# Kernel optimization log

Measured on AMD Instinct MI355X. Metric: run time of the kernel, lower is better.

## Reference

```python
import jax, jax.numpy as jnp
import numpy as np

T, B, D, H = 4096, 4, 1024, 8
EPS = 1e-5


def _ln(z, g, b):
    m = jnp.mean(z, axis=-1, keepdims=True)
    v = jnp.mean((z - m) ** 2, axis=-1, keepdims=True)
    return (z - m) * jax.lax.rsqrt(v + EPS) * g + b


def setup_inputs() -> dict:
    key = jax.random.key(0)
    ks = jax.random.split(key, 8)
    s = 0.02
    return {
        "x": jax.random.normal(ks[0], (T, B, D), dtype=jnp.float32),
        "norm_w": jnp.ones((D,), jnp.float32),
        "norm_b": jnp.zeros((D,), jnp.float32),
        "tnorm_w": jnp.ones((D,), jnp.float32),
        "tnorm_b": jnp.zeros((D,), jnp.float32),
        "Wq": jax.random.normal(ks[1], (D, D), jnp.float32) * s,
        "bq": jnp.zeros((D,), jnp.float32),
        "Wk": jax.random.normal(ks[2], (D, D), jnp.float32) * s,
        "bk": jnp.zeros((D,), jnp.float32),
        "Wv": jax.random.normal(ks[3], (D, D), jnp.float32) * s,
        "bv": jnp.zeros((D,), jnp.float32),
    }


def reference(x, norm_w, norm_b, tnorm_w, tnorm_b, Wq, bq, Wk, bk, Wv, bv):
    # x: (T, B, D) -> (B, T, D), matching torch x.permute(1, 0, 2)
    xb = jnp.transpose(x, (1, 0, 2))
    b, t, d = xb.shape
    hd = d // H
    xn = _ln(xb, norm_w, norm_b)          # query branch norm
    xtn = _ln(xb, tnorm_w, tnorm_b)       # key/value branch norm (text_norm applied to x)
    q = (xn @ Wq.T + bq).reshape(b, t, H, hd)
    k = (xtn @ Wk.T + bk).reshape(b, t, H, hd)
    v = (xtn @ Wv.T + bv).reshape(b, t, H, hd)
    q = jax.nn.softmax(q, axis=-1)        # softmax over head-dim
    k = jax.nn.softmax(k, axis=1)         # softmax over time
    # kv state: (B, H, hd, hd)
    att = jnp.einsum('bthd,bthl->bhdl', k, v)
    y = jnp.einsum('bthd,bhdl->bthl', q, att).reshape(b, t, d)
    return y  # original forward returns y directly (proj_out/dropout unused)
```

## Files before the change

kernel.cpp:

```cpp
#include <hip/hip_runtime.h>
#include <cstdint>

#define T_LEN 4096
#define BATCH 4
#define DIM   1024
#define NH    8
#define HDIM  128
#define ROWS  16384

typedef __bf16 bf16x8 __attribute__((ext_vector_type(8)));
typedef float  f32x4  __attribute__((ext_vector_type(4)));

__device__ __forceinline__ unsigned short f2bf(float f) {
  union { float f; unsigned u; } a; a.f = f;
  unsigned u = a.u;
  u += 0x7fff + ((u >> 16) & 1);
  return (unsigned short)(u >> 16);
}
__device__ __forceinline__ float bf2f(unsigned short h) {
  union { unsigned u; float f; } a; a.u = ((unsigned)h) << 16;
  return a.f;
}

__device__ __forceinline__ void gld_lds16(const unsigned short* g, unsigned short* l) {
  __builtin_amdgcn_global_load_lds(
      (const __attribute__((address_space(1))) unsigned int*)g,
      (__attribute__((address_space(3))) unsigned int*)l, 16, 0, 0);
}

__global__ __launch_bounds__(256) void lnw_kernel(
    const float* __restrict__ x, const float* __restrict__ nw, const float* __restrict__ nb,
    const float* __restrict__ tw, const float* __restrict__ tb,
    unsigned short* __restrict__ xn, unsigned short* __restrict__ xtn,
    const float* __restrict__ Wq, const float* __restrict__ Wk, const float* __restrict__ Wv,
    unsigned short* __restrict__ wbf) {
  int tid = threadIdx.x;
  if (blockIdx.x >= ROWS) {
    int i4 = (blockIdx.x - ROWS) * 256 + tid;
    int w = i4 >> 18;
    const float* src = (w == 0) ? Wq : (w == 1 ? Wk : Wv);
    float4 v = ((const float4*)src)[i4 & 262143];
    union { unsigned short u[4]; uint2 d; } o;
    o.u[0] = f2bf(v.x); o.u[1] = f2bf(v.y); o.u[2] = f2bf(v.z); o.u[3] = f2bf(v.w);
    ((uint2*)wbf)[i4] = o.d;
    return;
  }
  int row = blockIdx.x;
  int t = row >> 2, b = row & 3;
  const float4 v = ((const float4*)(x + (size_t)row * DIM))[tid];
  float s  = v.x + v.y + v.z + v.w;
  float s2 = v.x*v.x + v.y*v.y + v.z*v.z + v.w*v.w;
#pragma unroll
  for (int o = 32; o; o >>= 1) { s += __shfl_xor(s, o); s2 += __shfl_xor(s2, o); }
  __shared__ float red[8];
  int wv = tid >> 6;
  if ((tid & 63) == 0) { red[wv] = s; red[4 + wv] = s2; }
  __syncthreads();
  s  = red[0] + red[1] + red[2] + red[3];
  s2 = red[4] + red[5] + red[6] + red[7];
  float mean = s * (1.0f / DIM);
  float var  = s2 * (1.0f / DIM) - mean * mean;
  float rstd = rsqrtf(var + 1e-5f);
  size_t orow = ((size_t)b * T_LEN + t) * DIM;
  int c0 = tid * 4;
  float xv[4] = {v.x, v.y, v.z, v.w};
  union { unsigned short u[4]; uint2 d; } o1, o2;
#pragma unroll
  for (int j = 0; j < 4; ++j) {
    int c = c0 + j;
    float xh = (xv[j] - mean) * rstd;
    o1.u[j] = f2bf(xh * nw[c] + nb[c]);
    o2.u[j] = f2bf(xh * tw[c] + tb[c]);
  }
  *(uint2*)(xn  + orow + c0) = o1.d;
  *(uint2*)(xtn + orow + c0) = o2.d;
}

__global__ __launch_bounds__(512, 4) void qkv_gemm(
    const unsigned short* __restrict__ xn, const unsigned short* __restrict__ xtn,
    const unsigned short* __restrict__ wbf,
    const float* __restrict__ bq, const float* __restrict__ bk, const float* __restrict__ bv,
    unsigned short* __restrict__ qo, unsigned short* __restrict__ ko, unsigned short* __restrict__ vo,
    float* __restrict__ Zk) {
  int z = blockIdx.z;
  const unsigned short* A = (z == 0) ? xn : xtn;
  const unsigned short* W = wbf + (size_t)z * DIM * DIM;
  const float* bias = (z == 0) ? bq : (z == 1 ? bk : bv);
  unsigned short* outp = (z == 0) ? qo : (z == 1 ? ko : vo);

  int m0 = blockIdx.x * 256;
  int n0 = blockIdx.y * 128;

  __shared__ __align__(16) unsigned short lds[24576];

  int tid = threadIdx.x;
  int wave = tid >> 6, lane = tid & 63;
  int wr = wave >> 1, wc = wave & 1;
  int wm = wr * 64, wn = wc * 64;
  int l16 = lane & 15, kq = lane >> 4;
  int rs = (kq ^ ((l16 >> 1) & 3)) * 8;

  int arow = tid >> 2;
  int achk = (tid & 3) ^ ((tid >> 3) & 3);
  const unsigned short* Ag = A + (size_t)(m0 + arow) * DIM + achk * 8;
  const unsigned short* Wg = W + (size_t)(n0 + arow) * DIM + achk * 8;

  f32x4 acc[4][4] = {};

  auto stage = [&](int tt, int sb) {
    int kt = tt * 32;
    gld_lds16(Ag + kt,                     lds + sb + wave * 512);
    gld_lds16(Ag + (size_t)128 * DIM + kt, lds + sb + 4096 + wave * 512);
    gld_lds16(Wg + kt,                     lds + sb + 8192 + wave * 512);
  };

  stage(0, 0);
  stage(1, 12288);

  for (int t = 0; t < 32; ++t) {
    int sb = (t & 1) ? 12288 : 0;
    const unsigned short* As = lds + sb;
    const unsigned short* Bs = lds + sb + 8192;

    if (t < 31) asm volatile("s_waitcnt vmcnt(3)" ::: "memory");
    else        asm volatile("s_waitcnt vmcnt(0)" ::: "memory");
    __builtin_amdgcn_sched_barrier(0);
    __builtin_amdgcn_s_barrier();
    __builtin_amdgcn_sched_barrier(0);

    bf16x8 fa[4], fb[4];
#pragma unroll
    for (int i = 0; i < 4; ++i) {
      fa[i] = *(const bf16x8*)(As + (wm + i * 16 + l16) * 32 + rs);
      fb[i] = *(const bf16x8*)(Bs + (wn + i * 16 + l16) * 32 + rs);
    }
#pragma unroll
    for (int i = 0; i < 4; ++i)
#pragma unroll
      for (int j = 0; j < 4; ++j)
        acc[i][j] = __builtin_amdgcn_mfma_f32_16x16x32_bf16(fa[i], fb[j], acc[i][j], 0, 0, 0);

    __builtin_amdgcn_sched_barrier(0);
    __builtin_amdgcn_s_barrier();
    __builtin_amdgcn_sched_barrier(0);
    if (t < 30) stage(t + 2, sb);
    __builtin_amdgcn_sched_barrier(0);
  }

#pragma unroll
  for (int j = 0; j < 4; ++j) {
    float bc = bias[n0 + wn + j * 16 + l16];
#pragma unroll
    for (int i = 0; i < 4; ++i)
#pragma unroll
      for (int r = 0; r < 4; ++r) acc[i][j][r] += bc;
  }

  if (z == 0) {
    float* redm = (float*)lds;
    float* reds = redm + 512;
#pragma unroll
    for (int i = 0; i < 4; ++i) {
#pragma unroll
      for (int r = 0; r < 4; ++r) {
        float pm = acc[i][0][r];
#pragma unroll
        for (int j = 1; j < 4; ++j) pm = fmaxf(pm, acc[i][j][r]);
        pm = fmaxf(pm, __shfl_xor(pm, 1));
        pm = fmaxf(pm, __shfl_xor(pm, 2));
        pm = fmaxf(pm, __shfl_xor(pm, 4));
        pm = fmaxf(pm, __shfl_xor(pm, 8));
        float ps = 0.0f;
#pragma unroll
        for (int j = 0; j < 4; ++j) ps += __expf(acc[i][j][r] - pm);
        ps += __shfl_xor(ps, 1);
        ps += __shfl_xor(ps, 2);
        ps += __shfl_xor(ps, 4);
        ps += __shfl_xor(ps, 8);
        if (l16 == 0) {
          int row = wm + i * 16 + kq * 4 + r;
          redm[row * 2 + wc] = pm;
          reds[row * 2 + wc] = ps;
        }
      }
    }
    __syncthreads();
#pragma unroll
    for (int i = 0; i < 4; ++i) {
#pragma unroll
      for (int r = 0; r < 4; ++r) {
        int row = wm + i * 16 + kq * 4 + r;
        float ma = redm[row * 2], mb = redm[row * 2 + 1];
        float sa = reds[row * 2], sb2 = reds[row * 2 + 1];
        float M = fmaxf(ma, mb);
        float inv = 1.0f / (sa * __expf(ma - M) + sb2 * __expf(mb - M));
        size_t gr = (size_t)(m0 + row) * DIM;
#pragma unroll
        for (int j = 0; j < 4; ++j) {
          int col = n0 + wn + j * 16 + l16;
          outp[gr + col] = f2bf(__expf(acc[i][j][r] - M) * inv);
        }
      }
    }
  } else {
    int b = m0 >> 12;
    int tb = m0 & 4095;
    unsigned short* obase = outp + (size_t)b * DIM * T_LEN + tb;
    bool doExp = (z == 1);
    float zs[4] = {0.0f, 0.0f, 0.0f, 0.0f};
#pragma unroll
    for (int j = 0; j < 4; ++j) {
      int col = n0 + wn + j * 16 + l16;
      unsigned short* cp = obase + (size_t)col * T_LEN;
#pragma unroll
      for (int i = 0; i < 4; ++i) {
        int t0 = wm + i * 16 + kq * 4;
        union { unsigned short u[4]; uint2 d; } o;
#pragma unroll
        for (int r = 0; r < 4; ++r) {
          float val = acc[i][j][r];
          if (doExp) { val = __expf(val); zs[j] += val; }
          o.u[r] = f2bf(val);
        }
        *(uint2*)(cp + t0) = o.d;
      }
    }
    if (doExp) {
#pragma unroll
      for (int j = 0; j < 4; ++j) {
        zs[j] += __shfl_xor(zs[j], 16);
        zs[j] += __shfl_xor(zs[j], 32);
        if (kq == 0) {
          int col = n0 + wn + j * 16 + l16;
          atomicAdd(Zk + b * DIM + col, zs[j]);
        }
      }
    }
  }
}

__global__ __launch_bounds__(256) void att_gemm(
    const unsigned short* __restrict__ vT, const unsigned short* __restrict__ ksmT,
    float* __restrict__ slabs) {
  int kc = blockIdx.x;
  int bh = blockIdx.y;
  const unsigned short* Arow = vT   + (size_t)bh * HDIM * T_LEN;
  const unsigned short* Brow = ksmT + (size_t)bh * HDIM * T_LEN;
  __shared__ __align__(16) unsigned short As[128 * 64];
  __shared__ __align__(16) unsigned short Bs[128 * 64];
  int tid = threadIdx.x;
  int wave = tid >> 6, lane = tid & 63;
  int wm = (wave >> 1) * 64, wn = (wave & 1) * 64;
  int l16 = lane & 15, kq = lane >> 4;
  int swz = l16 & 7;
  int srow = tid >> 3;
  int skk = (((tid & 7) ^ ((tid >> 3) & 7)) * 8);
  const unsigned short* Ag = Arow + (size_t)srow * T_LEN + skk;
  const unsigned short* Bg = Brow + (size_t)srow * T_LEN + skk;
  unsigned short* Al = As + wave * 512;
  unsigned short* Bl = Bs + wave * 512;
  f32x4 acc[4][4] = {};
  int kbeg = kc * 256;
  for (int kt = kbeg; kt < kbeg + 256; kt += 64) {
#pragma unroll
    for (int p = 0; p < 4; ++p) {
      gld_lds16(Ag + (size_t)(p * 32) * T_LEN + kt, Al + p * 2048);
      gld_lds16(Bg + (size_t)(p * 32) * T_LEN + kt, Bl + p * 2048);
    }
    __syncthreads();
#pragma unroll
    for (int ks4 = 0; ks4 < 2; ++ks4) {
      int coff = (((kq + ks4 * 4) ^ swz) * 8);
      bf16x8 fa[4], fb[4];
#pragma unroll
      for (int i = 0; i < 4; ++i) {
        fa[i] = *(const bf16x8*)(As + (wm + i * 16 + l16) * 64 + coff);
        fb[i] = *(const bf16x8*)(Bs + (wn + i * 16 + l16) * 64 + coff);
      }
#pragma unroll
      for (int i = 0; i < 4; ++i)
#pragma unroll
        for (int j = 0; j < 4; ++j)
          acc[i][j] = __builtin_amdgcn_mfma_f32_16x16x32_bf16(fa[i], fb[j], acc[i][j], 0, 0, 0);
    }
    __syncthreads();
  }
  float* op = slabs + ((size_t)kc * 32 + bh) * 16384;
#pragma unroll
  for (int j = 0; j < 4; ++j) {
    int col = wn + j * 16 + l16;
#pragma unroll
    for (int i = 0; i < 4; ++i) {
      int rb = wm + i * 16 + kq * 4;
#pragma unroll
      for (int r = 0; r < 4; ++r)
        op[(size_t)(rb + r) * 128 + col] = acc[i][j][r];
    }
  }
}

__global__ __launch_bounds__(256) void attcvt(
    const float* __restrict__ slabs, const float* __restrict__ Zk,
    unsigned short* __restrict__ attbf) {
  int idx = blockIdx.x * 256 + threadIdx.x;
  int bh = idx >> 14;
  int b = bh >> 3, h = bh & 7;
  int d = idx & 127;
  float s = 0.0f;
#pragma unroll
  for (int kc = 0; kc < 16; ++kc) s += slabs[(size_t)kc * 524288 + idx];
  float zv = Zk[b * DIM + h * HDIM + d];
  attbf[idx] = f2bf(s / zv);
}

__global__ __launch_bounds__(256) void y_gemm(
    const unsigned short* __restrict__ qsm, const unsigned short* __restrict__ attbf,
    float* __restrict__ out) {
  int h = blockIdx.y;
  int m0t = blockIdx.x * 128;
  int b = m0t >> 12;
  int bh = b * 8 + h;
  const unsigned short* Brow = attbf + (size_t)bh * 16384;
  __shared__ __align__(16) unsigned short As[128 * 64];
  __shared__ __align__(16) unsigned short Bs[128 * 64];
  int tid = threadIdx.x;
  int wave = tid >> 6, lane = tid & 63;
  int wm = (wave >> 1) * 64, wn = (wave & 1) * 64;
  int l16 = lane & 15, kq = lane >> 4;
  int swz = l16 & 7;
  int srow = tid >> 3;
  int skk = (((tid & 7) ^ ((tid >> 3) & 7)) * 8);
  const unsigned short* Ag = qsm + (size_t)(m0t + srow) * DIM + h * HDIM + skk;
  const unsigned short* Bg = Brow + (size_t)srow * HDIM + skk;
  unsigned short* Al = As + wave * 512;
  unsigned short* Bl = Bs + wave * 512;
  f32x4 acc[4][4] = {};
  for (int kt = 0; kt < HDIM; kt += 64) {
#pragma unroll
    for (int p = 0; p < 4; ++p) {
      gld_lds16(Ag + (size_t)(p * 32) * DIM + kt, Al + p * 2048);
      gld_lds16(Bg + (size_t)(p * 32) * HDIM + kt, Bl + p * 2048);
    }
    __syncthreads();
#pragma unroll
    for (int ks4 = 0; ks4 < 2; ++ks4) {
      int coff = (((kq + ks4 * 4) ^ swz) * 8);
      bf16x8 fa[4], fb[4];
#pragma unroll
      for (int i = 0; i < 4; ++i) {
        fa[i] = *(const bf16x8*)(As + (wm + i * 16 + l16) * 64 + coff);
        fb[i] = *(const bf16x8*)(Bs + (wn + i * 16 + l16) * 64 + coff);
      }
#pragma unroll
      for (int i = 0; i < 4; ++i)
#pragma unroll
        for (int j = 0; j < 4; ++j)
          acc[i][j] = __builtin_amdgcn_mfma_f32_16x16x32_bf16(fa[i], fb[j], acc[i][j], 0, 0, 0);
    }
    __syncthreads();
  }
#pragma unroll
  for (int j = 0; j < 4; ++j) {
    int col = wn + j * 16 + l16;
#pragma unroll
    for (int i = 0; i < 4; ++i) {
      int rb = wm + i * 16 + kq * 4;
#pragma unroll
      for (int r = 0; r < 4; ++r)
        out[(size_t)(m0t + rb + r) * DIM + h * HDIM + col] = acc[i][j][r];
    }
  }
}

extern "C" void kernel_launch(void* const* d_in, const int* in_sizes, int n_in,
                              void* d_out, int out_size, void* d_ws, size_t ws_size,
                              hipStream_t stream) {
  const float* x  = (const float*)d_in[0];
  const float* nw = (const float*)d_in[1];
  const float* nb = (const float*)d_in[2];
  const float* tw = (const float*)d_in[3];
  const float* tb = (const float*)d_in[4];
  const float* Wq = (const float*)d_in[5];
  const float* bq = (const float*)d_in[6];
  const float* Wk = (const float*)d_in[7];
  const float* bk = (const float*)d_in[8];
  const float* Wv = (const float*)d_in[9];
  const float* bv = (const float*)d_in[10];
  float* out = (float*)d_out;

  char* ws = (char*)d_ws;
  unsigned short* xn   = (unsigned short*)(ws);
  unsigned short* xtn  = (unsigned short*)(ws + 33554432);
  unsigned short* q    = (unsigned short*)(ws + 67108864);
  unsigned short* ksmT = (unsigned short*)(ws + 100663296);
  unsigned short* vT   = (unsigned short*)(ws + 134217728);
  unsigned short* wbf  = (unsigned short*)(ws + 167772160);
  unsigned short* attbf= (unsigned short*)(ws + 176160768);
  float* Zk            = (float*)(ws + 177209344);
  float* slabs         = (float*)(ws);

  (void)hipMemsetAsync(Zk, 0, BATCH * DIM * 4, stream);
  lnw_kernel<<<ROWS + 3072, 256, 0, stream>>>(x, nw, nb, tw, tb, xn, xtn, Wq, Wk, Wv, wbf);
  qkv_gemm<<<dim3(64, 8, 3), 512, 0, stream>>>(xn, xtn, wbf, bq, bk, bv, q, ksmT, vT, Zk);
  att_gemm<<<dim3(16, 32), 256, 0, stream>>>(vT, ksmT, slabs);
  attcvt<<<2048, 256, 0, stream>>>(slabs, Zk, attbf);
  y_gemm<<<dim3(128, 8), 256, 0, stream>>>(q, attbf, out);
}
```

Measured before the change: 317.3 us.

## Fuse Q projection and softmax into the y GEMM, drop q round-trip

```diff
diff --git a/kernel.cpp b/kernel.cpp
--- a/kernel.cpp
+++ b/kernel.cpp
@@ -76,17 +76,15 @@
   *(uint2*)(xtn + orow + c0) = o2.d;
 }
 
-__global__ __launch_bounds__(512, 4) void qkv_gemm(
-    const unsigned short* __restrict__ xn, const unsigned short* __restrict__ xtn,
-    const unsigned short* __restrict__ wbf,
-    const float* __restrict__ bq, const float* __restrict__ bk, const float* __restrict__ bv,
-    unsigned short* __restrict__ qo, unsigned short* __restrict__ ko, unsigned short* __restrict__ vo,
+__global__ __launch_bounds__(512, 4) void kv_gemm(
+    const unsigned short* __restrict__ xtn, const unsigned short* __restrict__ wbf,
+    const float* __restrict__ bk, const float* __restrict__ bv,
+    unsigned short* __restrict__ ko, unsigned short* __restrict__ vo,
     float* __restrict__ Zk) {
-  int z = blockIdx.z;
-  const unsigned short* A = (z == 0) ? xn : xtn;
-  const unsigned short* W = wbf + (size_t)z * DIM * DIM;
-  const float* bias = (z == 0) ? bq : (z == 1 ? bk : bv);
-  unsigned short* outp = (z == 0) ? qo : (z == 1 ? ko : vo);
+  int zz = blockIdx.z + 1;
+  const unsigned short* W = wbf + (size_t)zz * DIM * DIM;
+  const float* bias = (zz == 1) ? bk : bv;
+  unsigned short* outp = (zz == 1) ? ko : vo;
 
   int m0 = blockIdx.x * 256;
   int n0 = blockIdx.y * 128;
@@ -102,7 +100,7 @@
 
   int arow = tid >> 2;
   int achk = (tid & 3) ^ ((tid >> 3) & 3);
-  const unsigned short* Ag = A + (size_t)(m0 + arow) * DIM + achk * 8;
+  const unsigned short* Ag = xtn + (size_t)(m0 + arow) * DIM + achk * 8;
   const unsigned short* Wg = W + (size_t)(n0 + arow) * DIM + achk * 8;
 
   f32x4 acc[4][4] = {};
@@ -156,84 +154,36 @@
       for (int r = 0; r < 4; ++r) acc[i][j][r] += bc;
   }
 
-  if (z == 0) {
-    float* redm = (float*)lds;
-    float* reds = redm + 512;
-#pragma unroll
-    for (int i = 0; i < 4; ++i) {
+  int b = m0 >> 12;
+  int tb = m0 & 4095;
+  unsigned short* obase = outp + (size_t)b * DIM * T_LEN + tb;
+  bool doExp = (zz == 1);
+  float zs[4] = {0.0f, 0.0f, 0.0f, 0.0f};
+#pragma unroll
+  for (int j = 0; j < 4; ++j) {
+    int col = n0 + wn + j * 16 + l16;
+    unsigned short* cp = obase + (size_t)col * T_LEN;
+#pragma unroll
+    for (int i = 0; i < 4; ++i) {
+      int t0 = wm + i * 16 + kq * 4;
+      union { unsigned short u[4]; uint2 d; } o;
 #pragma unroll
       for (int r = 0; r < 4; ++r) {
-        float pm = acc[i][0][r];
-#pragma unroll
-        for (int j = 1; j < 4; ++j) pm = fmaxf(pm, acc[i][j][r]);
-        pm = fmaxf(pm, __shfl_xor(pm, 1));
-        pm = fmaxf(pm, __shfl_xor(pm, 2));
-        pm = fmaxf(pm, __shfl_xor(pm, 4));
-        pm = fmaxf(pm, __shfl_xor(pm, 8));
-        float ps = 0.0f;
-#pragma unroll
-        for (int j = 0; j < 4; ++j) ps += __expf(acc[i][j][r] - pm);
-        ps += __shfl_xor(ps, 1);
-        ps += __shfl_xor(ps, 2);
-        ps += __shfl_xor(ps, 4);
-        ps += __shfl_xor(ps, 8);
-        if (l16 == 0) {
-          int row = wm + i * 16 + kq * 4 + r;
-          redm[row * 2 + wc] = pm;
-          reds[row * 2 + wc] = ps;
-        }
-      }
-    }
-    __syncthreads();
-#pragma unroll
-    for (int i = 0; i < 4; ++i) {
-#pragma unroll
-      for (int r = 0; r < 4; ++r) {
-        int row = wm + i * 16 + kq * 4 + r;
-        float ma = redm[row * 2], mb = redm[row * 2 + 1];
-        float sa = reds[row * 2], sb2 = reds[row * 2 + 1];
-        float M = fmaxf(ma, mb);
-        float inv = 1.0f / (sa * __expf(ma - M) + sb2 * __expf(mb - M));
-        size_t gr = (size_t)(m0 + row) * DIM;
-#pragma unroll
-        for (int j = 0; j < 4; ++j) {
-          int col = n0 + wn + j * 16 + l16;
-          outp[gr + col] = f2bf(__expf(acc[i][j][r] - M) * inv);
-        }
-      }
-    }
-  } else {
-    int b = m0 >> 12;
-    int tb = m0 & 4095;
-    unsigned short* obase = outp + (size_t)b * DIM * T_LEN + tb;
-    bool doExp = (z == 1);
-    float zs[4] = {0.0f, 0.0f, 0.0f, 0.0f};
+        float val = acc[i][j][r];
+        if (doExp) { val = __expf(val); zs[j] += val; }
+        o.u[r] = f2bf(val);
+      }
+      *(uint2*)(cp + t0) = o.d;
+    }
+  }
+  if (doExp) {
 #pragma unroll
     for (int j = 0; j < 4; ++j) {
-      int col = n0 + wn + j * 16 + l16;
-      unsigned short* cp = obase + (size_t)col * T_LEN;
-#pragma unroll
-      for (int i = 0; i < 4; ++i) {
-        int t0 = wm + i * 16 + kq * 4;
-        union { unsigned short u[4]; uint2 d; } o;
-#pragma unroll
-        for (int r = 0; r < 4; ++r) {
-          float val = acc[i][j][r];
-          if (doExp) { val = __expf(val); zs[j] += val; }
-          o.u[r] = f2bf(val);
-        }
-        *(uint2*)(cp + t0) = o.d;
-      }
-    }
-    if (doExp) {
-#pragma unroll
-      for (int j = 0; j < 4; ++j) {
-        zs[j] += __shfl_xor(zs[j], 16);
-        zs[j] += __shfl_xor(zs[j], 32);
-        if (kq == 0) {
-          int col = n0 + wn + j * 16 + l16;
-          atomicAdd(Zk + b * DIM + col, zs[j]);
-        }
+      zs[j] += __shfl_xor(zs[j], 16);
+      zs[j] += __shfl_xor(zs[j], 32);
+      if (kq == 0) {
+        int col = n0 + wn + j * 16 + l16;
+        atomicAdd(Zk + b * DIM + col, zs[j]);
       }
     }
   }
@@ -260,8 +210,8 @@
   unsigned short* Al = As + wave * 512;
   unsigned short* Bl = Bs + wave * 512;
   f32x4 acc[4][4] = {};
-  int kbeg = kc * 256;
-  for (int kt = kbeg; kt < kbeg + 256; kt += 64) {
+  int kbeg = kc * 512;
+  for (int kt = kbeg; kt < kbeg + 512; kt += 64) {
 #pragma unroll
     for (int p = 0; p < 4; ++p) {
       gld_lds16(Ag + (size_t)(p * 32) * T_LEN + kt, Al + p * 2048);
@@ -308,66 +258,184 @@
   int d = idx & 127;
   float s = 0.0f;
 #pragma unroll
-  for (int kc = 0; kc < 16; ++kc) s += slabs[(size_t)kc * 524288 + idx];
+  for (int kc = 0; kc < 8; ++kc) s += slabs[(size_t)kc * 524288 + idx];
   float zv = Zk[b * DIM + h * HDIM + d];
   attbf[idx] = f2bf(s / zv);
 }
 
-__global__ __launch_bounds__(256) void y_gemm(
-    const unsigned short* __restrict__ qsm, const unsigned short* __restrict__ attbf,
+__global__ __launch_bounds__(512) void qy_gemm(
+    const unsigned short* __restrict__ xn, const unsigned short* __restrict__ wbf,
+    const float* __restrict__ bq, const unsigned short* __restrict__ attbf,
     float* __restrict__ out) {
-  int h = blockIdx.y;
-  int m0t = blockIdx.x * 128;
-  int b = m0t >> 12;
+  int m0 = blockIdx.x * 256;
+  int h  = blockIdx.y;
+  int n0 = h * HDIM;
+  int b  = m0 >> 12;
   int bh = b * 8 + h;
-  const unsigned short* Brow = attbf + (size_t)bh * 16384;
-  __shared__ __align__(16) unsigned short As[128 * 64];
-  __shared__ __align__(16) unsigned short Bs[128 * 64];
+
+  __shared__ __align__(16) unsigned short lds[24576];
+
   int tid = threadIdx.x;
   int wave = tid >> 6, lane = tid & 63;
-  int wm = (wave >> 1) * 64, wn = (wave & 1) * 64;
+  int wr = wave >> 1, wc = wave & 1;
+  int wm = wr * 64, wn = wc * 64;
   int l16 = lane & 15, kq = lane >> 4;
-  int swz = l16 & 7;
-  int srow = tid >> 3;
-  int skk = (((tid & 7) ^ ((tid >> 3) & 7)) * 8);
-  const unsigned short* Ag = qsm + (size_t)(m0t + srow) * DIM + h * HDIM + skk;
-  const unsigned short* Bg = Brow + (size_t)srow * HDIM + skk;
-  unsigned short* Al = As + wave * 512;
-  unsigned short* Bl = Bs + wave * 512;
+  int rs = (kq ^ ((l16 >> 1) & 3)) * 8;
+
+  int arow = tid >> 2;
+  int achk = (tid & 3) ^ ((tid >> 3) & 3);
+  const unsigned short* Ag = xn + (size_t)(m0 + arow) * DIM + achk * 8;
+  const unsigned short* Wg = wbf + (size_t)(n0 + arow) * DIM + achk * 8;
+
   f32x4 acc[4][4] = {};
-  for (int kt = 0; kt < HDIM; kt += 64) {
-#pragma unroll
-    for (int p = 0; p < 4; ++p) {
-      gld_lds16(Ag + (size_t)(p * 32) * DIM + kt, Al + p * 2048);
-      gld_lds16(Bg + (size_t)(p * 32) * HDIM + kt, Bl + p * 2048);
+
+  auto stage = [&](int tt, int sb) {
+    int kt = tt * 32;
+    gld_lds16(Ag + kt,                     lds + sb + wave * 512);
+    gld_lds16(Ag + (size_t)128 * DIM + kt, lds + sb + 4096 + wave * 512);
+    gld_lds16(Wg + kt,                     lds + sb + 8192 + wave * 512);
+  };
+
+  stage(0, 0);
+  stage(1, 12288);
+
+  for (int t = 0; t < 32; ++t) {
+    int sb = (t & 1) ? 12288 : 0;
+    const unsigned short* As = lds + sb;
+    const unsigned short* Bs = lds + sb + 8192;
+
+    if (t < 31) asm volatile("s_waitcnt vmcnt(3)" ::: "memory");
+    else        asm volatile("s_waitcnt vmcnt(0)" ::: "memory");
+    __builtin_amdgcn_sched_barrier(0);
+    __builtin_amdgcn_s_barrier();
+    __builtin_amdgcn_sched_barrier(0);
+
+    bf16x8 fa[4], fb[4];
+#pragma unroll
+    for (int i = 0; i < 4; ++i) {
+      fa[i] = *(const bf16x8*)(As + (wm + i * 16 + l16) * 32 + rs);
+      fb[i] = *(const bf16x8*)(Bs + (wn + i * 16 + l16) * 32 + rs);
+    }
+#pragma unroll
+    for (int i = 0; i < 4; ++i)
+#pragma unroll
+      for (int j = 0; j < 4; ++j)
+        acc[i][j] = __builtin_amdgcn_mfma_f32_16x16x32_bf16(fa[i], fb[j], acc[i][j], 0, 0, 0);
+
+    __builtin_amdgcn_sched_barrier(0);
+    __builtin_amdgcn_s_barrier();
+    __builtin_amdgcn_sched_barrier(0);
+    if (t < 30) stage(t + 2, sb);
+    __builtin_amdgcn_sched_barrier(0);
+  }
+
+#pragma unroll
+  for (int j = 0; j < 4; ++j) {
+    float bc = bq[n0 + wn + j * 16 + l16];
+#pragma unroll
+    for (int i = 0; i < 4; ++i)
+#pragma unroll
+      for (int r = 0; r < 4; ++r) acc[i][j][r] += bc;
+  }
+
+  int wmy = (wave >> 2) * 64, wny = (wave & 3) * 32;
+  bf16x8 fby[2][4];
+#pragma unroll
+  for (int jy = 0; jy < 2; ++jy)
+#pragma unroll
+    for (int ks = 0; ks < 4; ++ks) {
+      int ncol = wny + jy * 16 + l16;
+      fby[jy][ks] = *(const bf16x8*)(attbf + (size_t)bh * 16384 + ncol * 128 + ks * 32 + kq * 8);
+    }
+
+  {
+    float* redm = (float*)lds;
+    float* reds = redm + 512;
+#pragma unroll
+    for (int i = 0; i < 4; ++i) {
+#pragma unroll
+      for (int r = 0; r < 4; ++r) {
+        float pm = acc[i][0][r];
+#pragma unroll
+        for (int j = 1; j < 4; ++j) pm = fmaxf(pm, acc[i][j][r]);
+        pm = fmaxf(pm, __shfl_xor(pm, 1));
+        pm = fmaxf(pm, __shfl_xor(pm, 2));
+        pm = fmaxf(pm, __shfl_xor(pm, 4));
+        pm = fmaxf(pm, __shfl_xor(pm, 8));
+        float ps = 0.0f;
+#pragma unroll
+        for (int j = 0; j < 4; ++j) ps += __expf(acc[i][j][r] - pm);
+        ps += __shfl_xor(ps, 1);
+        ps += __shfl_xor(ps, 2);
+        ps += __shfl_xor(ps, 4);
+        ps += __shfl_xor(ps, 8);
+        if (l16 == 0) {
+          int row = wm + i * 16 + kq * 4 + r;
+          redm[row * 2 + wc] = pm;
+          reds[row * 2 + wc] = ps;
+        }
+      }
     }
     __syncthreads();
 #pragma unroll
-    for (int ks4 = 0; ks4 < 2; ++ks4) {
-      int coff = (((kq + ks4 * 4) ^ swz) * 8);
-      bf16x8 fa[4], fb[4];
-#pragma unroll
-      for (int i = 0; i < 4; ++i) {
-        fa[i] = *(const bf16x8*)(As + (wm + i * 16 + l16) * 64 + coff);
-        fb[i] = *(const bf16x8*)(Bs + (wn + i * 16 + l16) * 64 + coff);
-      }
+    for (int i = 0; i < 4; ++i) {
+#pragma unroll
+      for (int r = 0; r < 4; ++r) {
+        int row = wm + i * 16 + kq * 4 + r;
+        float ma = redm[row * 2], mb = redm[row * 2 + 1];
+        float sa = reds[row * 2], sb2 = reds[row * 2 + 1];
+        float M = fmaxf(ma, mb);
+        float inv = 1.0f / (sa * __expf(ma - M) + sb2 * __expf(mb - M));
+#pragma unroll
+        for (int j = 0; j < 4; ++j)
+          acc[i][j][r] = __expf(acc[i][j][r] - M) * inv;
+      }
+    }
+  }
+
+#pragma unroll
+  for (int p = 0; p < 2; ++p) {
+    __syncthreads();
+    if ((wr >> 1) == p) {
+      int wmL = wm - p * 128;
 #pragma unroll
       for (int i = 0; i < 4; ++i)
 #pragma unroll
-        for (int j = 0; j < 4; ++j)
-          acc[i][j] = __builtin_amdgcn_mfma_f32_16x16x32_bf16(fa[i], fb[j], acc[i][j], 0, 0, 0);
+        for (int j = 0; j < 4; ++j) {
+          int col = wn + j * 16 + l16;
+#pragma unroll
+          for (int r = 0; r < 4; ++r) {
+            int row = wmL + i * 16 + kq * 4 + r;
+            lds[row * 136 + col] = f2bf(acc[i][j][r]);
+          }
+        }
     }
     __syncthreads();
-  }
-#pragma unroll
-  for (int j = 0; j < 4; ++j) {
-    int col = wn + j * 16 + l16;
-#pragma unroll
-    for (int i = 0; i < 4; ++i) {
-      int rb = wm + i * 16 + kq * 4;
-#pragma unroll
-      for (int r = 0; r < 4; ++r)
-        out[(size_t)(m0t + rb + r) * DIM + h * HDIM + col] = acc[i][j][r];
+    f32x4 accy[4][2] = {};
+#pragma unroll
+    for (int ks = 0; ks < 4; ++ks) {
+      bf16x8 fay[4];
+#pragma unroll
+      for (int iy = 0; iy < 4; ++iy) {
+        int row = wmy + iy * 16 + l16;
+        fay[iy] = *(const bf16x8*)(lds + row * 136 + ks * 32 + kq * 8);
+      }
+#pragma unroll
+      for (int iy = 0; iy < 4; ++iy)
+#pragma unroll
+        for (int jy = 0; jy < 2; ++jy)
+          accy[iy][jy] = __builtin_amdgcn_mfma_f32_16x16x32_bf16(fay[iy], fby[jy][ks], accy[iy][jy], 0, 0, 0);
+    }
+#pragma unroll
+    for (int jy = 0; jy < 2; ++jy) {
+      int colg = n0 + wny + jy * 16 + l16;
+#pragma unroll
+      for (int iy = 0; iy < 4; ++iy) {
+        int rowg = m0 + p * 128 + wmy + iy * 16 + kq * 4;
+#pragma unroll
+        for (int r = 0; r < 4; ++r)
+          out[(size_t)(rowg + r) * DIM + colg] = accy[iy][jy][r];
+      }
     }
   }
 }
@@ -391,18 +459,17 @@
   char* ws = (char*)d_ws;
   unsigned short* xn   = (unsigned short*)(ws);
   unsigned short* xtn  = (unsigned short*)(ws + 33554432);
-  unsigned short* q    = (unsigned short*)(ws + 67108864);
+  float* slabs         = (float*)(ws + 67108864);
   unsigned short* ksmT = (unsigned short*)(ws + 100663296);
   unsigned short* vT   = (unsigned short*)(ws + 134217728);
   unsigned short* wbf  = (unsigned short*)(ws + 167772160);
   unsigned short* attbf= (unsigned short*)(ws + 176160768);
   float* Zk            = (float*)(ws + 177209344);
-  float* slabs         = (float*)(ws);
 
   (void)hipMemsetAsync(Zk, 0, BATCH * DIM * 4, stream);
   lnw_kernel<<<ROWS + 3072, 256, 0, stream>>>(x, nw, nb, tw, tb, xn, xtn, Wq, Wk, Wv, wbf);
-  qkv_gemm<<<dim3(64, 8, 3), 512, 0, stream>>>(xn, xtn, wbf, bq, bk, bv, q, ksmT, vT, Zk);
-  att_gemm<<<dim3(16, 32), 256, 0, stream>>>(vT, ksmT, slabs);
+  kv_gemm<<<dim3(64, 8, 2), 512, 0, stream>>>(xtn, wbf, bk, bv, ksmT, vT, Zk);
+  att_gemm<<<dim3(8, 32), 256, 0, stream>>>(vT, ksmT, slabs);
   attcvt<<<2048, 256, 0, stream>>>(slabs, Zk, attbf);
-  y_gemm<<<dim3(128, 8), 256, 0, stream>>>(q, attbf, out);
-}
+  qy_gemm<<<dim3(64, 8), 512, 0, stream>>>(xn, wbf, bq, attbf, out);
+}
```

New measurement: 330.3 us. 1.04x slower.
